# Kernel tuning notes

Measured on AMD Instinct MI355X. Metric: run time of the kernel, lower is better.

## Reference

```python
import jax, jax.numpy as jnp
import numpy as np

TEMPERATURE = 0.07
NUM_HARD_NEGATIVES = 5
BATCH, DIM = 4096, 768


def setup_inputs() -> dict:
    key = jax.random.key(0)
    k1, k2 = jax.random.split(key)
    return {
        "text_emb": jax.random.normal(k1, (BATCH, DIM), dtype=jnp.float32),
        "table_emb": jax.random.normal(k2, (BATCH, DIM), dtype=jnp.float32),
    }


def _ttcl_loss(text_emb, table_emb):
    # F.normalize(dim=1)
    t = text_emb / jnp.linalg.norm(text_emb, axis=1, keepdims=True)
    z = table_emb / jnp.linalg.norm(table_emb, axis=1, keepdims=True)
    sim = z @ t.T  # [B, B], sim[i, j] = <table_i, text_j>
    B = sim.shape[0]
    pos = jnp.diagonal(sim) / TEMPERATURE  # [B], <text_i, table_i> == <table_i, text_i>
    diag_mask = jnp.eye(B, dtype=bool)
    neg_inf = jnp.finfo(sim.dtype).min

    def hard_neg_loss(neg_rows):
        # neg_rows[i] holds the B candidate negatives for sample i; exclude self.
        neg = jnp.where(diag_mask, neg_inf, neg_rows)
        top_vals, _ = jax.lax.top_k(neg, NUM_HARD_NEGATIVES)  # [B, k]
        logits = jnp.concatenate([pos[:, None], top_vals / TEMPERATURE], axis=1)  # [B, k+1]
        # cross_entropy with label 0 == -log_softmax(logits)[:, 0]
        return -jax.nn.log_softmax(logits, axis=1)[:, 0]

    # t2z: negatives for i are sim[j][i], j != i  -> column i -> rows of sim.T
    loss_t2z = jnp.sum(hard_neg_loss(sim.T))
    # z2t: negatives for i are sim[i][j], j != i  -> row i
    loss_z2t = jnp.sum(hard_neg_loss(sim))
    loss = (loss_t2z + loss_z2t) / (2 * B)
    return loss, sim


def reference(text_emb, table_emb):
    return _ttcl_loss(text_emb, table_emb)
```

## Files before the change

kernel.cpp:

```cpp
#include <hip/hip_runtime.h>
#include <stdint.h>
#include <math.h>

#define BSZ 4096
#define DIM 768
#define TEMP 0.07f

typedef short short8 __attribute__((ext_vector_type(8)));
typedef float f32x4 __attribute__((ext_vector_type(4)));


__device__ __forceinline__ uint16_t f2bf(float f) {
  uint32_t u = __float_as_uint(f);
  uint32_t r = (u + 0x7FFFu + ((u >> 16) & 1u)) >> 16;
  return (uint16_t)r;
}

__device__ __forceinline__ void gll16(const void* g, void* l) {
  __builtin_amdgcn_global_load_lds(
      (__attribute__((address_space(1))) void*)(uintptr_t)g,
      (__attribute__((address_space(3))) void*)l,
      16, 0, 0);
}

__device__ __forceinline__ void ins5(float v, float& a, float& b, float& c,
                                     float& d, float& e) {
  if (v > e) {
    e = v;
    if (e > d) { float t = d; d = e; e = t;
      if (d > c) { t = c; c = d; d = t;
        if (c > b) { t = b; b = c; c = t;
          if (b > a) { t = a; a = b; b = t; } } } }
  }
}

__device__ __forceinline__ void sins5(float v, float& a, float& b, float& c,
                                      float& d, float& e) {
  float t;
  t = fmaxf(a, v); v = fminf(a, v); a = t;
  t = fmaxf(b, v); v = fminf(b, v); b = t;
  t = fmaxf(c, v); v = fminf(c, v); c = t;
  t = fmaxf(d, v); v = fminf(d, v); d = t;
  e = fmaxf(e, v);
}

__global__ __launch_bounds__(256) void k_norm(const float* __restrict__ text,
                                              const float* __restrict__ table,
                                              uint16_t* __restrict__ tn,
                                              uint16_t* __restrict__ zn) {
  int row = blockIdx.x & (BSZ - 1);
  bool isTable = blockIdx.x >= BSZ;
  const float* src = (isTable ? table : text) + (size_t)row * DIM;
  uint16_t* dst = (isTable ? zn : tn) + (size_t)row * DIM;
  int tid = threadIdx.x;

  float x0 = src[tid];
  float x1 = src[tid + 256];
  float x2 = src[tid + 512];
  float ss = x0 * x0 + x1 * x1 + x2 * x2;
  #pragma unroll
  for (int off = 32; off >= 1; off >>= 1) ss += __shfl_xor(ss, off);
  __shared__ float wss[4];
  if ((tid & 63) == 0) wss[tid >> 6] = ss;
  __syncthreads();
  float inv = rsqrtf(wss[0] + wss[1] + wss[2] + wss[3]);
  dst[tid]       = f2bf(x0 * inv);
  dst[tid + 256] = f2bf(x1 * inv);
  dst[tid + 512] = f2bf(x2 * inv);
}

__global__ __launch_bounds__(512, 2) void k_gemm(const uint16_t* __restrict__ Zb,
                                                 const uint16_t* __restrict__ Tb,
                                                 float* __restrict__ sim) {
  extern __shared__ __attribute__((aligned(16))) char lds[];

  int tid = threadIdx.x;
  int wave = tid >> 6, lane = tid & 63;
  int wm = wave >> 2, wn = wave & 3;
  int brow = (blockIdx.x >> 4) << 8;
  int bcol = (blockIdx.x & 15) << 8;

  f32x4 acc[8][4] = {};

  const uint16_t* gA = Zb + (size_t)brow * DIM + wave * 8;
  const uint16_t* gB = Tb + (size_t)bcol * DIM + wave * 8;
  char* ldsA = lds + (wave << 12);

  int kqg = lane >> 4;
  int rbyte = ((wm << 7) + (lane & 15)) << 4;
  int cbyte = ((wn << 6) + (lane & 15)) << 4;

  auto SA = [&](int t2, int bb, int rg) {
    gll16(gA + (size_t)t2 * 64 + (size_t)(rg * 64 + lane) * DIM,
          ldsA + bb + rg * 1024);
  };
  auto SB = [&](int t2, int bb, int rg) {
    gll16(gB + (size_t)t2 * 64 + (size_t)(rg * 64 + lane) * DIM,
          ldsA + bb + 32768 + rg * 1024);
  };

  auto LOADB = [&](int bb, short8 (&bf)[2][4]) {
    #pragma unroll
    for (int ks = 0; ks < 2; ++ks) {
      const char* Bb = lds + bb + (((ks << 2) + kqg) << 12) + 32768;
      #pragma unroll
      for (int n = 0; n < 4; ++n)
        bf[ks][n] = *(const short8*)(Bb + cbyte + (n << 8));
    }
  };
  auto PHASE = [&](int bb, int mlo, short8 (&bf)[2][4]) {
    __builtin_amdgcn_s_setprio(1);
    #pragma unroll
    for (int ks = 0; ks < 2; ++ks) {
      const char* Ab = lds + bb + (((ks << 2) + kqg) << 12);
      #pragma unroll
      for (int m = 0; m < 4; ++m) {
        short8 af = *(const short8*)(Ab + rbyte + ((mlo + m) << 8));
        #pragma unroll
        for (int n = 0; n < 4; ++n)
          acc[mlo + m][n] = __builtin_amdgcn_mfma_f32_16x16x32_bf16(
              af, bf[ks][n], acc[mlo + m][n], 0, 0, 0);
      }
    }
    __builtin_amdgcn_s_setprio(0);
  };

  #pragma unroll
  for (int rg = 0; rg < 4; ++rg) { SA(0, 0, rg); SB(0, 0, rg); }
  #pragma unroll
  for (int rg = 0; rg < 4; ++rg) { SA(1, 65536, rg); SB(1, 65536, rg); }
  asm volatile("s_waitcnt vmcnt(8)" ::: "memory");
  __builtin_amdgcn_s_barrier();

  #pragma unroll 2
  for (int t = 0; t < 10; ++t) {
    int bb = (t & 1) << 16;
    short8 bf[2][4];
    LOADB(bb, bf);
    PHASE(bb, 0, bf);
    __builtin_amdgcn_s_barrier();
    SA(t + 2, bb, 0); SA(t + 2, bb, 2);
    SB(t + 2, bb, 0); SB(t + 2, bb, 1); SB(t + 2, bb, 2); SB(t + 2, bb, 3);
    PHASE(bb, 4, bf);
    __builtin_amdgcn_s_barrier();
    SA(t + 2, bb, 1); SA(t + 2, bb, 3);
    asm volatile("s_waitcnt vmcnt(8)" ::: "memory");
    __builtin_amdgcn_s_barrier();
  }

  {
    short8 bf[2][4];
    LOADB(0, bf);
    PHASE(0, 0, bf);
    PHASE(0, 4, bf);
  }
  asm volatile("s_waitcnt vmcnt(0)" ::: "memory");
  __builtin_amdgcn_s_barrier();
  {
    short8 bf[2][4];
    LOADB(65536, bf);
    PHASE(65536, 0, bf);
    PHASE(65536, 4, bf);
  }

  int crow0 = brow + (wm << 7) + ((lane >> 4) << 2);
  int ccol0 = bcol + (wn << 6) + (lane & 15);
  #pragma unroll
  for (int m = 0; m < 8; ++m)
    #pragma unroll
    for (int n = 0; n < 4; ++n)
      #pragma unroll
      for (int r = 0; r < 4; ++r)
        sim[(size_t)(crow0 + m * 16 + r) * BSZ + (ccol0 + n * 16)] = acc[m][n][r];
}

__global__ __launch_bounds__(256) void k_tile(const float* __restrict__ sim,
                                              float* __restrict__ rp,
                                              float* __restrict__ cp) {
  extern __shared__ float l32[];
  int tid = threadIdx.x;
  int tr = blockIdx.x >> 5, tc = blockIdx.x & 31;
  int row0 = tr << 7, col0 = tc << 7;
  bool diag = (tr == tc);

  int q = tid & 31;
  int g = tid >> 5;
  const float* gsrc = sim + (size_t)(row0 + (g << 4)) * BSZ + col0 + (q << 2);

  f32x4 v[16];
  #pragma unroll
  for (int k = 0; k < 16; ++k)
    v[k] = *(const f32x4*)(gsrc + (size_t)k * BSZ);

  #pragma unroll
  for (int k = 0; k < 16; ++k) {
    int r = (g << 4) + k;
    if (diag && (r >> 2) == q) v[k][r & 3] = -1e30f;
    *(f32x4*)(l32 + (r << 7) + ((q ^ (r & 7)) << 2)) = v[k];
  }
  __syncthreads();

  {
    int row = tid >> 1, h = tid & 1;
    int rx = row & 7;
    const float* rb = l32 + (row << 7);
    float a0 = -1e30f, a1 = -1e30f, a2 = -1e30f, a3 = -1e30f, a4 = -1e30f;
    #pragma unroll
    for (int j = 0; j < 16; ++j) {
      int c16 = (h << 4) + j;
      f32x4 x = *(const f32x4*)(rb + ((c16 ^ rx) << 2));
      sins5(x[0], a0, a1, a2, a3, a4);
      sins5(x[1], a0, a1, a2, a3, a4);
      sins5(x[2], a0, a1, a2, a3, a4);
      sins5(x[3], a0, a1, a2, a3, a4);
    }
    float b0 = __shfl_xor(a0, 1), b1 = __shfl_xor(a1, 1),
          b2 = __shfl_xor(a2, 1), b3 = __shfl_xor(a3, 1),
          b4 = __shfl_xor(a4, 1);
    sins5(b0, a0, a1, a2, a3, a4);
    sins5(b1, a0, a1, a2, a3, a4);
    sins5(b2, a0, a1, a2, a3, a4);
    sins5(b3, a0, a1, a2, a3, a4);
    sins5(b4, a0, a1, a2, a3, a4);
    if (h == 0) {
      float* pr = rp + ((size_t)(row0 + row) * 32 + tc) * 5;
      pr[0] = a0; pr[1] = a1; pr[2] = a2; pr[3] = a3; pr[4] = a4;
    }
  }

  {
    int c = tid >> 1, hf = tid & 1;
    int cc = c >> 2, cw = c & 3;
    float a0 = -1e30f, a1 = -1e30f, a2 = -1e30f, a3 = -1e30f, a4 = -1e30f;
    #pragma unroll 8
    for (int k = 0; k < 64; ++k) {
      int r = (hf << 6) + k;
      float x = l32[(r << 7) + (((cc ^ (r & 7)) << 2) | cw)];
      sins5(x, a0, a1, a2, a3, a4);
    }
    float b0 = __shfl_xor(a0, 1), b1 = __shfl_xor(a1, 1),
          b2 = __shfl_xor(a2, 1), b3 = __shfl_xor(a3, 1),
          b4 = __shfl_xor(a4, 1);
    sins5(b0, a0, a1, a2, a3, a4);
    sins5(b1, a0, a1, a2, a3, a4);
    sins5(b2, a0, a1, a2, a3, a4);
    sins5(b3, a0, a1, a2, a3, a4);
    sins5(b4, a0, a1, a2, a3, a4);
    if (hf == 0) {
      float* pc = cp + ((size_t)(col0 + c) * 32 + tr) * 5;
      pc[0] = a0; pc[1] = a1; pc[2] = a2; pc[3] = a3; pc[4] = a4;
    }
  }
}

__global__ __launch_bounds__(256) void k_merge(const float* __restrict__ sim,
                                               const float* __restrict__ rp,
                                               const float* __restrict__ cp,
                                               float* __restrict__ lossbuf) {
  int wave = threadIdx.x >> 6, lane = threadIdx.x & 63;
  int wid = blockIdx.x * 4 + wave;
  bool isCol = wid >= BSZ;
  int line = isCol ? wid - BSZ : wid;
  const float* src = (isCol ? cp : rp) + (size_t)line * 160;

  float t0 = -1e30f, t1 = -1e30f, t2 = -1e30f, t3 = -1e30f, t4 = -1e30f;
  ins5(src[lane], t0, t1, t2, t3, t4);
  ins5(src[lane + 64], t0, t1, t2, t3, t4);
  if (lane < 32) ins5(src[lane + 128], t0, t1, t2, t3, t4);

  float top[5];
  #pragma unroll
  for (int e = 0; e < 5; e++) {
    float m = t0;
    #pragma unroll
    for (int off = 32; off >= 1; off >>= 1) m = fmaxf(m, __shfl_xor(m, off));
    unsigned long long msk = __ballot(t0 == m);
    int owner = __ffsll(msk) - 1;
    if (lane == owner) { t0 = t1; t1 = t2; t2 = t3; t3 = t4; t4 = -1e30f; }
    top[e] = m;
  }

  if (lane == 0) {
    float pos = sim[(size_t)line * BSZ + line] / TEMP;
    float l0 = top[0] / TEMP, l1 = top[1] / TEMP, l2 = top[2] / TEMP,
          l3 = top[3] / TEMP, l4 = top[4] / TEMP;
    float mx = fmaxf(pos, fmaxf(fmaxf(l0, l1), fmaxf(fmaxf(l2, l3), l4)));
    float s = expf(pos - mx) + expf(l0 - mx) + expf(l1 - mx) +
              expf(l2 - mx) + expf(l3 - mx) + expf(l4 - mx);
    lossbuf[wid] = mx + logf(s) - pos;
  }
}

__global__ __launch_bounds__(256) void k_reduce(const float* __restrict__ losses,
                                                float* __restrict__ out) {
  int tid = threadIdx.x;
  float s = 0.f;
  for (int i = tid; i < 2 * BSZ; i += 256) s += losses[i];
  #pragma unroll
  for (int off = 32; off >= 1; off >>= 1) s += __shfl_xor(s, off);
  __shared__ float wss[4];
  if ((tid & 63) == 0) wss[tid >> 6] = s;
  __syncthreads();
  if (tid == 0) out[0] = (wss[0] + wss[1] + wss[2] + wss[3]) / (2.0f * BSZ);
}

extern "C" void kernel_launch(void* const* d_in, const int* in_sizes, int n_in,
                              void* d_out, int out_size, void* d_ws, size_t ws_size,
                              hipStream_t stream) {
  const float* text = (const float*)d_in[0];
  const float* table = (const float*)d_in[1];
  float* out = (float*)d_out;
  float* sim = out + 1;

  uint16_t* Zb = (uint16_t*)d_ws;
  uint16_t* Tb = Zb + (size_t)BSZ * DIM;
  float* lossbuf = (float*)(Tb + (size_t)BSZ * DIM);

  float* rp = (float*)d_ws;
  float* cp = rp + (size_t)BSZ * 32 * 5;

  k_norm<<<2 * BSZ, 256, 0, stream>>>(text, table, Tb, Zb);
  k_gemm<<<(BSZ / 256) * (BSZ / 256), 512, 131072, stream>>>(Zb, Tb, sim);
  k_tile<<<32 * 32, 256, 65536, stream>>>(sim, rp, cp);
  k_merge<<<2 * BSZ / 4, 256, 0, stream>>>(sim, rp, cp, lossbuf);
  k_reduce<<<1, 256, 0, stream>>>(lossbuf, out);
}
```

Measured before the change: 89.17 us.

## Shrink GEMM tiles to 128x128 with XCD-aware block swizzle

The sim GEMM moves from 256x256 tiles with 512 threads and 128KB LDS to 128x128 tiles with 256 threads and 64KB LDS, giving 1024 blocks instead of 256. Block indices are remapped so each XCD works on a contiguous region of the output, which should improve L2 reuse of the A and B panels. The A-row LDS layout uses a permuted position mapping to fit the new staging pattern. Smaller tiles give more parallelism and occupancy across the CUs, at the cost of lower arithmetic intensity and more global re-reads of the inputs.

```diff
diff --git a/kernel.cpp b/kernel.cpp
--- a/kernel.cpp
+++ b/kernel.cpp
@@ -69,40 +69,52 @@
   dst[tid + 512] = f2bf(x2 * inv);
 }
 
-__global__ __launch_bounds__(512, 2) void k_gemm(const uint16_t* __restrict__ Zb,
+__global__ __launch_bounds__(256, 2) void k_gemm(const uint16_t* __restrict__ Zb,
                                                  const uint16_t* __restrict__ Tb,
                                                  float* __restrict__ sim) {
   extern __shared__ __attribute__((aligned(16))) char lds[];
 
   int tid = threadIdx.x;
   int wave = tid >> 6, lane = tid & 63;
-  int wm = wave >> 2, wn = wave & 3;
-  int brow = (blockIdx.x >> 4) << 8;
-  int bcol = (blockIdx.x & 15) << 8;
-
-  f32x4 acc[8][4] = {};
-
-  const uint16_t* gA = Zb + (size_t)brow * DIM + wave * 8;
-  const uint16_t* gB = Tb + (size_t)bcol * DIM + wave * 8;
-  char* ldsA = lds + (wave << 12);
-
+  int wm = wave >> 1, wn = wave & 1;
+
+  int bid = blockIdx.x;
+  int xcd = bid & 7, li = bid >> 3;
+  int trow = ((xcd >> 2) << 4) + (li >> 3);
+  int tcol = ((xcd & 3) << 3) + (li & 7);
+  int brow = trow << 7, bcol = tcol << 7;
+
+  f32x4 acc[4][4] = {};
+
+  const uint16_t* gA = Zb + (size_t)brow * DIM;
+  const uint16_t* gB = Tb + (size_t)bcol * DIM;
+
+  int c0 = wave, c1 = wave + 4;
+  int rA0 = (lane & 31) | ((lane & 32) << 1);
   int kqg = lane >> 4;
-  int rbyte = ((wm << 7) + (lane & 15)) << 4;
   int cbyte = ((wn << 6) + (lane & 15)) << 4;
 
-  auto SA = [&](int t2, int bb, int rg) {
-    gll16(gA + (size_t)t2 * 64 + (size_t)(rg * 64 + lane) * DIM,
-          ldsA + bb + rg * 1024);
-  };
-  auto SB = [&](int t2, int bb, int rg) {
-    gll16(gB + (size_t)t2 * 64 + (size_t)(rg * 64 + lane) * DIM,
-          ldsA + bb + 32768 + rg * 1024);
+  int rbyteM[4];
+  #pragma unroll
+  for (int m = 0; m < 4; ++m) {
+    int row = (wm << 6) + (m << 4) + (lane & 15);
+    int pos = (row & 31) | ((row & 32) << 1) | ((row & 64) >> 1);
+    rbyteM[m] = pos << 4;
+  }
+
+  auto SA = [&](int t, int bb, int c, int u) {
+    gll16(gA + (size_t)(rA0 + u * 32) * DIM + t * 64 + c * 8,
+          lds + bb + (c << 11) + (u << 10));
+  };
+  auto SB = [&](int t, int bb, int c, int u) {
+    gll16(gB + (size_t)((u << 6) + lane) * DIM + t * 64 + c * 8,
+          lds + bb + 16384 + (c << 11) + (u << 10));
   };
 
   auto LOADB = [&](int bb, short8 (&bf)[2][4]) {
     #pragma unroll
     for (int ks = 0; ks < 2; ++ks) {
-      const char* Bb = lds + bb + (((ks << 2) + kqg) << 12) + 32768;
+      const char* Bb = lds + bb + 16384 + (((ks << 2) + kqg) << 11);
       #pragma unroll
       for (int n = 0; n < 4; ++n)
         bf[ks][n] = *(const short8*)(Bb + cbyte + (n << 8));
@@ -112,38 +124,43 @@
     __builtin_amdgcn_s_setprio(1);
     #pragma unroll
     for (int ks = 0; ks < 2; ++ks) {
-      const char* Ab = lds + bb + (((ks << 2) + kqg) << 12);
+      const char* Ab = lds + bb + (((ks << 2) + kqg) << 11);
       #pragma unroll
-      for (int m = 0; m < 4; ++m) {
-        short8 af = *(const short8*)(Ab + rbyte + ((mlo + m) << 8));
+      for (int mm = 0; mm < 2; ++mm) {
+        int m = mlo + mm;
+        short8 af = *(const short8*)(Ab + rbyteM[m]);
         #pragma unroll
         for (int n = 0; n < 4; ++n)
-          acc[mlo + m][n] = __builtin_amdgcn_mfma_f32_16x16x32_bf16(
-              af, bf[ks][n], acc[mlo + m][n], 0, 0, 0);
+          acc[m][n] = __builtin_amdgcn_mfma_f32_16x16x32_bf16(
+              af, bf[ks][n], acc[m][n], 0, 0, 0);
       }
     }
     __builtin_amdgcn_s_setprio(0);
   };
 
-  #pragma unroll
-  for (int rg = 0; rg < 4; ++rg) { SA(0, 0, rg); SB(0, 0, rg); }
-  #pragma unroll
-  for (int rg = 0; rg < 4; ++rg) { SA(1, 65536, rg); SB(1, 65536, rg); }
+  auto STAGEALL = [&](int t, int bb) {
+    SA(t, bb, c0, 0); SA(t, bb, c0, 1); SA(t, bb, c1, 0); SA(t, bb, c1, 1);
+    SB(t, bb, c0, 0); SB(t, bb, c0, 1); SB(t, bb, c1, 0); SB(t, bb, c1, 1);
+  };
+
+  STAGEALL(0, 0);
+  STAGEALL(1, 32768);
   asm volatile("s_waitcnt vmcnt(8)" ::: "memory");
   __builtin_amdgcn_s_barrier();
 
   #pragma unroll 2
   for (int t = 0; t < 10; ++t) {
-    int bb = (t & 1) << 16;
+    int bb = (t & 1) << 15;
     short8 bf[2][4];
     LOADB(bb, bf);
     PHASE(bb, 0, bf);
     __builtin_amdgcn_s_barrier();
-    SA(t + 2, bb, 0); SA(t + 2, bb, 2);
-    SB(t + 2, bb, 0); SB(t + 2, bb, 1); SB(t + 2, bb, 2); SB(t + 2, bb, 3);
-    PHASE(bb, 4, bf);
+    SA(t + 2, bb, c0, 0); SA(t + 2, bb, c1, 0);
+    SB(t + 2, bb, c0, 0); SB(t + 2, bb, c0, 1);
+    SB(t + 2, bb, c1, 0); SB(t + 2, bb, c1, 1);
+    PHASE(bb, 2, bf);
     __builtin_amdgcn_s_barrier();
-    SA(t + 2, bb, 1); SA(t + 2, bb, 3);
+    SA(t + 2, bb, c0, 1); SA(t + 2, bb, c1, 1);
     asm volatile("s_waitcnt vmcnt(8)" ::: "memory");
     __builtin_amdgcn_s_barrier();
   }
@@ -152,21 +169,21 @@
     short8 bf[2][4];
     LOADB(0, bf);
     PHASE(0, 0, bf);
-    PHASE(0, 4, bf);
+    PHASE(0, 2, bf);
   }
   asm volatile("s_waitcnt vmcnt(0)" ::: "memory");
   __builtin_amdgcn_s_barrier();
   {
     short8 bf[2][4];
-    LOADB(65536, bf);
-    PHASE(65536, 0, bf);
-    PHASE(65536, 4, bf);
-  }
-
-  int crow0 = brow + (wm << 7) + ((lane >> 4) << 2);
+    LOADB(32768, bf);
+    PHASE(32768, 0, bf);
+    PHASE(32768, 2, bf);
+  }
+
+  int crow0 = brow + (wm << 6) + ((lane >> 4) << 2);
   int ccol0 = bcol + (wn << 6) + (lane & 15);
   #pragma unroll
-  for (int m = 0; m < 8; ++m)
+  for (int m = 0; m < 4; ++m)
     #pragma unroll
     for (int n = 0; n < 4; ++n)
       #pragma unroll
@@ -320,7 +337,7 @@
   float* cp = rp + (size_t)BSZ * 32 * 5;
 
   k_norm<<<2 * BSZ, 256, 0, stream>>>(text, table, Tb, Zb);
-  k_gemm<<<(BSZ / 256) * (BSZ / 256), 512, 131072, stream>>>(Zb, Tb, sim);
+  k_gemm<<<(BSZ / 128) * (BSZ / 128), 256, 65536, stream>>>(Zb, Tb, sim);
   k_tile<<<32 * 32, 256, 65536, stream>>>(sim, rp, cp);
   k_merge<<<2 * BSZ / 4, 256, 0, stream>>>(sim, rp, cp, lossbuf);
   k_reduce<<<1, 256, 0, stream>>>(lossbuf, out);
```

Result: slower. 103.9 us (+16.5%).

## Split GEMM main loop into four sub-phases with interleaved async loads

Applied to the files above, without the earlier changes.

Restructures the bf16 MFMA GEMM main loop so that each K-tile is processed in four sub-phases. Each sub-phase explicitly reads A fragments from LDS, waits on lgkmcnt, and then runs its MFMAs. Global-to-LDS loads for future tiles are spread across the sub-phases, and the A row-group 1/3 loads are moved into the next tile's start. The goal is finer overlap of LDS reads, global loads and MFMA, but it adds more barriers per tile and the loop is no longer unrolled.

```diff
diff --git a/kernel.cpp b/kernel.cpp
--- a/kernel.cpp
+++ b/kernel.cpp
@@ -84,19 +84,19 @@
 
   const uint16_t* gA = Zb + (size_t)brow * DIM + wave * 8;
   const uint16_t* gB = Tb + (size_t)bcol * DIM + wave * 8;
-  char* ldsA = lds + (wave << 12);
+  char* ldsW = lds + (wave << 12);
 
   int kqg = lane >> 4;
   int rbyte = ((wm << 7) + (lane & 15)) << 4;
   int cbyte = ((wn << 6) + (lane & 15)) << 4;
 
-  auto SA = [&](int t2, int bb, int rg) {
-    gll16(gA + (size_t)t2 * 64 + (size_t)(rg * 64 + lane) * DIM,
-          ldsA + bb + rg * 1024);
-  };
-  auto SB = [&](int t2, int bb, int rg) {
-    gll16(gB + (size_t)t2 * 64 + (size_t)(rg * 64 + lane) * DIM,
-          ldsA + bb + 32768 + rg * 1024);
+  auto SA = [&](int t, int bb, int rg) {
+    gll16(gA + (size_t)t * 64 + (size_t)(rg * 64 + lane) * DIM,
+          ldsW + bb + rg * 1024);
+  };
+  auto SB = [&](int t, int bb, int rg) {
+    gll16(gB + (size_t)t * 64 + (size_t)(rg * 64 + lane) * DIM,
+          ldsW + bb + 32768 + rg * 1024);
   };
 
   auto LOADB = [&](int bb, short8 (&bf)[2][4]) {
@@ -108,21 +108,55 @@
         bf[ks][n] = *(const short8*)(Bb + cbyte + (n << 8));
     }
   };
-  auto PHASE = [&](int bb, int mlo, short8 (&bf)[2][4]) {
-    __builtin_amdgcn_s_setprio(1);
+  auto AREAD = [&](int bb, int mp, short8 (&af)[2][2]) {
     #pragma unroll
     for (int ks = 0; ks < 2; ++ks) {
       const char* Ab = lds + bb + (((ks << 2) + kqg) << 12);
+      af[ks][0] = *(const short8*)(Ab + rbyte + (((mp << 1) + 0) << 8));
+      af[ks][1] = *(const short8*)(Ab + rbyte + (((mp << 1) + 1) << 8));
+    }
+  };
+  auto MM = [&](int mp, short8 (&af)[2][2], short8 (&bf)[2][4]) {
+    __builtin_amdgcn_s_setprio(1);
+    #pragma unroll
+    for (int ks = 0; ks < 2; ++ks)
       #pragma unroll
-      for (int m = 0; m < 4; ++m) {
-        short8 af = *(const short8*)(Ab + rbyte + ((mlo + m) << 8));
+      for (int mm = 0; mm < 2; ++mm)
         #pragma unroll
         for (int n = 0; n < 4; ++n)
-          acc[mlo + m][n] = __builtin_amdgcn_mfma_f32_16x16x32_bf16(
-              af, bf[ks][n], acc[mlo + m][n], 0, 0, 0);
-      }
-    }
+          acc[(mp << 1) + mm][n] = __builtin_amdgcn_mfma_f32_16x16x32_bf16(
+              af[ks][mm], bf[ks][n], acc[(mp << 1) + mm][n], 0, 0, 0);
     __builtin_amdgcn_s_setprio(0);
+  };
+
+#define LGKM0_BAR                                          \
+  __builtin_amdgcn_s_barrier();                            \
+  asm volatile("s_waitcnt lgkmcnt(0)" ::: "memory");
+
+  auto TILE = [&](int t, int bb, bool s0, bool s12, int vm) {
+    short8 bf[2][4], af[2][2];
+    LOADB(bb, bf);
+    AREAD(bb, 0, af);
+    if (s0) { SA(t + 1, bb ^ 65536, 1); SA(t + 1, bb ^ 65536, 3); }
+    LGKM0_BAR;
+    MM(0, af, bf);
+    __builtin_amdgcn_s_barrier();
+    AREAD(bb, 1, af);
+    if (s12) { SB(t + 2, bb, 0); SB(t + 2, bb, 1); SB(t + 2, bb, 2); SB(t + 2, bb, 3); }
+    LGKM0_BAR;
+    MM(1, af, bf);
+    __builtin_amdgcn_s_barrier();
+    AREAD(bb, 2, af);
+    if (s12) { SA(t + 2, bb, 0); SA(t + 2, bb, 2); }
+    LGKM0_BAR;
+    MM(2, af, bf);
+    __builtin_amdgcn_s_barrier();
+    AREAD(bb, 3, af);
+    LGKM0_BAR;
+    MM(3, af, bf);
+    if (vm == 6) asm volatile("s_waitcnt vmcnt(6)" ::: "memory");
+    else if (vm == 0) asm volatile("s_waitcnt vmcnt(0)" ::: "memory");
+    __builtin_amdgcn_s_barrier();
   };
 
   #pragma unroll
@@ -132,36 +166,13 @@
   asm volatile("s_waitcnt vmcnt(8)" ::: "memory");
   __builtin_amdgcn_s_barrier();
 
-  #pragma unroll 2
-  for (int t = 0; t < 10; ++t) {
-    int bb = (t & 1) << 16;
-    short8 bf[2][4];
-    LOADB(bb, bf);
-    PHASE(bb, 0, bf);
-    __builtin_amdgcn_s_barrier();
-    SA(t + 2, bb, 0); SA(t + 2, bb, 2);
-    SB(t + 2, bb, 0); SB(t + 2, bb, 1); SB(t + 2, bb, 2); SB(t + 2, bb, 3);
-    PHASE(bb, 4, bf);
-    __builtin_amdgcn_s_barrier();
-    SA(t + 2, bb, 1); SA(t + 2, bb, 3);
-    asm volatile("s_waitcnt vmcnt(8)" ::: "memory");
-    __builtin_amdgcn_s_barrier();
-  }
-
-  {
-    short8 bf[2][4];
-    LOADB(0, bf);
-    PHASE(0, 0, bf);
-    PHASE(0, 4, bf);
-  }
-  asm volatile("s_waitcnt vmcnt(0)" ::: "memory");
-  __builtin_amdgcn_s_barrier();
-  {
-    short8 bf[2][4];
-    LOADB(65536, bf);
-    PHASE(65536, 0, bf);
-    PHASE(65536, 4, bf);
-  }
+  TILE(0, 0, false, true, 6);
+  #pragma unroll 1
+  for (int t = 1; t <= 9; ++t) TILE(t, (t & 1) << 16, true, true, 6);
+  TILE(10, 0, true, false, 0);
+  TILE(11, 65536, false, false, -1);
+
+#undef LGKM0_BAR
 
   int crow0 = brow + (wm << 7) + ((lane >> 4) << 2);
   int ccol0 = bcol + (wn << 6) + (lane & 15);
```

New measurement: 89.42 us. Within noise of the previous version (+0.3%).

## Shrink GEMM tile to 128x128 with 4 waves and simple double-buffered K loop

Applied to the files above, without the earlier changes.

Replaces the 256x256 tile, 8-wave GEMM that used a two-phase interleaved prefetch schedule with a 128x128 tile, 4-wave kernel. The new kernel stages K=32 slices into a 32KB double buffer with one barrier per step. The smaller tile gives 1024 blocks instead of 256, filling the CUs better, and the lower LDS and register footprint permits more resident blocks. In exchange, each block reuses loaded data less, so global/L2 traffic rises, and the finer per-K-step barrier cadence with 24 iterations may expose more latency.

```diff
diff --git a/kernel.cpp b/kernel.cpp
--- a/kernel.cpp
+++ b/kernel.cpp
@@ -69,104 +69,68 @@
   dst[tid + 512] = f2bf(x2 * inv);
 }
 
-__global__ __launch_bounds__(512, 2) void k_gemm(const uint16_t* __restrict__ Zb,
+__global__ __launch_bounds__(256, 3) void k_gemm(const uint16_t* __restrict__ Zb,
                                                  const uint16_t* __restrict__ Tb,
                                                  float* __restrict__ sim) {
   extern __shared__ __attribute__((aligned(16))) char lds[];
 
   int tid = threadIdx.x;
   int wave = tid >> 6, lane = tid & 63;
-  int wm = wave >> 2, wn = wave & 3;
-  int brow = (blockIdx.x >> 4) << 8;
-  int bcol = (blockIdx.x & 15) << 8;
-
-  f32x4 acc[8][4] = {};
+  int wm = wave >> 1, wn = wave & 1;
+  int brow = (blockIdx.x >> 5) << 7;
+  int bcol = (blockIdx.x & 31) << 7;
+
+  f32x4 acc[4][4] = {};
 
   const uint16_t* gA = Zb + (size_t)brow * DIM + wave * 8;
   const uint16_t* gB = Tb + (size_t)bcol * DIM + wave * 8;
-  char* ldsA = lds + (wave << 12);
+  char* ldsW = lds + (wave << 11);
 
   int kqg = lane >> 4;
-  int rbyte = ((wm << 7) + (lane & 15)) << 4;
+  int rbyte = ((wm << 6) + (lane & 15)) << 4;
   int cbyte = ((wn << 6) + (lane & 15)) << 4;
 
-  auto SA = [&](int t2, int bb, int rg) {
-    gll16(gA + (size_t)t2 * 64 + (size_t)(rg * 64 + lane) * DIM,
-          ldsA + bb + rg * 1024);
+  auto STAGE = [&](int t, int bb) {
+    const uint16_t* a = gA + (size_t)t * 32;
+    const uint16_t* b = gB + (size_t)t * 32;
+    gll16(a + (size_t)lane * DIM,        ldsW + bb);
+    gll16(a + (size_t)(64 + lane) * DIM, ldsW + bb + 1024);
+    gll16(b + (size_t)lane * DIM,        ldsW + bb + 8192);
+    gll16(b + (size_t)(64 + lane) * DIM, ldsW + bb + 8192 + 1024);
   };
-  auto SB = [&](int t2, int bb, int rg) {
-    gll16(gB + (size_t)t2 * 64 + (size_t)(rg * 64 + lane) * DIM,
-          ldsA + bb + 32768 + rg * 1024);
-  };
-
-  auto LOADB = [&](int bb, short8 (&bf)[2][4]) {
-    #pragma unroll
-    for (int ks = 0; ks < 2; ++ks) {
-      const char* Bb = lds + bb + (((ks << 2) + kqg) << 12) + 32768;
+
+  auto COMPUTE = [&](int bb) {
+    const char* Ab = lds + bb + (kqg << 11);
+    const char* Bb = Ab + 8192;
+    short8 af[4], bf[4];
+    #pragma unroll
+    for (int m = 0; m < 4; ++m)
+      af[m] = *(const short8*)(Ab + rbyte + (m << 8));
+    #pragma unroll
+    for (int n = 0; n < 4; ++n)
+      bf[n] = *(const short8*)(Bb + cbyte + (n << 8));
+    #pragma unroll
+    for (int m = 0; m < 4; ++m)
       #pragma unroll
       for (int n = 0; n < 4; ++n)
-        bf[ks][n] = *(const short8*)(Bb + cbyte + (n << 8));
-    }
+        acc[m][n] = __builtin_amdgcn_mfma_f32_16x16x32_bf16(
+            af[m], bf[n], acc[m][n], 0, 0, 0);
   };
-  auto PHASE = [&](int bb, int mlo, short8 (&bf)[2][4]) {
-    __builtin_amdgcn_s_setprio(1);
-    #pragma unroll
-    for (int ks = 0; ks < 2; ++ks) {
-      const char* Ab = lds + bb + (((ks << 2) + kqg) << 12);
-      #pragma unroll
-      for (int m = 0; m < 4; ++m) {
-        short8 af = *(const short8*)(Ab + rbyte + ((mlo + m) << 8));
-        #pragma unroll
-        for (int n = 0; n < 4; ++n)
-          acc[mlo + m][n] = __builtin_amdgcn_mfma_f32_16x16x32_bf16(
-              af, bf[ks][n], acc[mlo + m][n], 0, 0, 0);
-      }
-    }
-    __builtin_amdgcn_s_setprio(0);
-  };
-
-  #pragma unroll
-  for (int rg = 0; rg < 4; ++rg) { SA(0, 0, rg); SB(0, 0, rg); }
-  #pragma unroll
-  for (int rg = 0; rg < 4; ++rg) { SA(1, 65536, rg); SB(1, 65536, rg); }
-  asm volatile("s_waitcnt vmcnt(8)" ::: "memory");
-  __builtin_amdgcn_s_barrier();
-
+
+  STAGE(0, 0);
+  __syncthreads();
   #pragma unroll 2
-  for (int t = 0; t < 10; ++t) {
-    int bb = (t & 1) << 16;
-    short8 bf[2][4];
-    LOADB(bb, bf);
-    PHASE(bb, 0, bf);
-    __builtin_amdgcn_s_barrier();
-    SA(t + 2, bb, 0); SA(t + 2, bb, 2);
-    SB(t + 2, bb, 0); SB(t + 2, bb, 1); SB(t + 2, bb, 2); SB(t + 2, bb, 3);
-    PHASE(bb, 4, bf);
-    __builtin_amdgcn_s_barrier();
-    SA(t + 2, bb, 1); SA(t + 2, bb, 3);
-    asm volatile("s_waitcnt vmcnt(8)" ::: "memory");
-    __builtin_amdgcn_s_barrier();
-  }
-
-  {
-    short8 bf[2][4];
-    LOADB(0, bf);
-    PHASE(0, 0, bf);
-    PHASE(0, 4, bf);
-  }
-  asm volatile("s_waitcnt vmcnt(0)" ::: "memory");
-  __builtin_amdgcn_s_barrier();
-  {
-    short8 bf[2][4];
-    LOADB(65536, bf);
-    PHASE(65536, 0, bf);
-    PHASE(65536, 4, bf);
-  }
-
-  int crow0 = brow + (wm << 7) + ((lane >> 4) << 2);
+  for (int t = 0; t < 23; ++t) {
+    STAGE(t + 1, ((t + 1) & 1) << 14);
+    COMPUTE((t & 1) << 14);
+    __syncthreads();
+  }
+  COMPUTE(16384);
+
+  int crow0 = brow + (wm << 6) + ((lane >> 4) << 2);
   int ccol0 = bcol + (wn << 6) + (lane & 15);
   #pragma unroll
-  for (int m = 0; m < 8; ++m)
+  for (int m = 0; m < 4; ++m)
     #pragma unroll
     for (int n = 0; n < 4; ++n)
       #pragma unroll
@@ -320,7 +284,7 @@
   float* cp = rp + (size_t)BSZ * 32 * 5;
 
   k_norm<<<2 * BSZ, 256, 0, stream>>>(text, table, Tb, Zb);
-  k_gemm<<<(BSZ / 256) * (BSZ / 256), 512, 131072, stream>>>(Zb, Tb, sim);
+  k_gemm<<<(BSZ / 128) * (BSZ / 128), 256, 32768, stream>>>(Zb, Tb, sim);
   k_tile<<<32 * 32, 256, 65536, stream>>>(sim, rp, cp);
   k_merge<<<2 * BSZ / 4, 256, 0, stream>>>(sim, rp, cp, lossbuf);
   k_reduce<<<1, 256, 0, stream>>>(lossbuf, out);
```

After: 106.3 us. +19.2%, slower.
